# Kernel tuning notes

Measured on AMD Instinct MI355X. Metric: run time of the kernel, lower is better.

The kernel has to match this reference:

```python
import jax, jax.numpy as jnp
import numpy as np

BIG = 1e10  # sentinel for invalid pairwise distances


def get_xyz(depth, fx, fy, cx, cy):
    # depth: [B,1,H,W] -> xyz: [B,3,H,W] via pinhole unprojection
    B, _, H, W = depth.shape
    v = jnp.arange(H, dtype=depth.dtype)[:, None]   # rows
    u = jnp.arange(W, dtype=depth.dtype)[None, :]   # cols
    z = depth[:, 0]                                  # [B,H,W]
    x = (u - cx) / fx * z
    y = (v - cy) / fy * z
    return jnp.stack([x, y, z], axis=1)              # [B,3,H,W]


def _chamfer_item(p, g, vp, vg):
    # p,g: [N,3] point sets; vp,vg: [N] bool validity masks
    # squared pairwise distances via ||p||^2 + ||g||^2 - 2 p.g
    d = (jnp.sum(p * p, -1)[:, None] + jnp.sum(g * g, -1)[None, :]
         - 2.0 * (p @ g.T))                          # [N,N]
    d = jnp.maximum(d, 0.0)
    has_g = jnp.any(vg)
    has_p = jnp.any(vp)
    d1 = jnp.min(jnp.where(vg[None, :], d, BIG), axis=1)  # per pred point
    d2 = jnp.min(jnp.where(vp[:, None], d, BIG), axis=0)  # per gt point
    s1 = jnp.sum(jnp.where(vp & has_g, d1, 0.0))
    s2 = jnp.sum(jnp.where(vg & has_p, d2, 0.0))
    return s1 + s2


def reference(pred, gt_xyz, mask, fx, fy, cx, cy):
    B = pred.shape[0]
    pred_xyz = get_xyz(pred, fx, fy, cx, cy)             # [B,3,H,W]
    p = pred_xyz.reshape(B, 3, -1).transpose(0, 2, 1)    # [B,N,3]
    g = gt_xyz.reshape(B, 3, -1).transpose(0, 2, 1)      # [B,N,3]
    m = mask[:, 0].reshape(B, -1) > 0                    # [B,N]
    # ignore_zeros=True: drop points whose coordinate sum is exactly 0
    vp = m & (jnp.sum(p, -1) != 0)
    vg = m & (jnp.sum(g, -1) != 0)
    per_item = jax.vmap(_chamfer_item)(p, g, vp, vg)     # [B]
    return jnp.sum(per_item) / B


def setup_inputs() -> dict:
    key = jax.random.key(0)
    k1, k2, k3 = jax.random.split(key, 3)
    B, H, W = 2, 128, 128
    pred = jax.random.uniform(k1, (B, 1, H, W), dtype=jnp.float32) * 2.0 + 0.1
    gt_xyz = jax.random.normal(k2, (B, 3, H, W), dtype=jnp.float32)
    mask = jax.random.randint(k3, (B, 1, H, W), 0, 2, dtype=jnp.int32)
    fx = jnp.float32(525.0)
    fy = jnp.float32(525.0)
    cx = jnp.float32(64.0)
    cy = jnp.float32(64.0)
    return {"pred": pred, "gt_xyz": gt_xyz, "mask": mask,
            "fx": fx, "fy": fy, "cx": cx, "cy": cy}
```

## Files before the change

kernel.cpp:

```cpp
#include <hip/hip_runtime.h>

#define B_ITEMS 2
#define W_IMG   128
#define N_PTS   16384
#define CH_GRID 1024

__global__ __launch_bounds__(256) void prep_kernel(
        const float* __restrict__ pred,
        const float* __restrict__ gt,
        const int*   __restrict__ mask,
        const float* fxp, const float* fyp,
        const float* cxp, const float* cyp,
        int*    __restrict__ cnt,
        float4* __restrict__ pR, float4* __restrict__ gR,
        float4* __restrict__ pT, float4* __restrict__ gT,
        float*  __restrict__ out) {
    int s    = blockIdx.x >> 6;
    int b    = s & 1;
    int isG  = s >> 1;
    int tid  = threadIdx.x;
    int idx  = (blockIdx.x & 63) * 256 + tid;
    int lane = tid & 63, w = tid >> 6;

    if (blockIdx.x == 0 && tid == 0) out[0] = 0.0f;

    float x, y, z;
    if (!isG) {
        float fx = *fxp, fy = *fyp, cx = *cxp, cy = *cyp;
        float u = (float)(idx & (W_IMG - 1));
        float v = (float)(idx >> 7);
        z = pred[b * N_PTS + idx];
        x = (u - cx) / fx * z;
        y = (v - cy) / fy * z;
    } else {
        x = gt[(b * 3 + 0) * N_PTS + idx];
        y = gt[(b * 3 + 1) * N_PTS + idx];
        z = gt[(b * 3 + 2) * N_PTS + idx];
    }
    int  mv = mask[b * N_PTS + idx];
    bool ok = (mv > 0) && (((x + y) + z) != 0.0f);

    unsigned long long bal = __ballot(ok);
    int nw  = __popcll(bal);
    int pre = __popcll(bal & ((1ull << lane) - 1ull));

    __shared__ int wbase[4];
    __shared__ int blockbase;
    if (lane == 0) wbase[w] = nw;
    __syncthreads();
    if (tid == 0) {
        int s0 = 0;
#pragma unroll
        for (int i = 0; i < 4; ++i) { int t = wbase[i]; wbase[i] = s0; s0 += t; }
        blockbase = s0 ? atomicAdd(&cnt[s], s0) : 0;
    }
    __syncthreads();

    if (ok) {
        int pos = blockbase + wbase[w] + pre;
        float ps = fmaf(z, z, fmaf(y, y, x * x));
        float4* __restrict__ raw = (isG ? gR : pR) + b * N_PTS;
        float4* __restrict__ tf  = (isG ? gT : pT) + b * N_PTS;
        raw[pos] = make_float4(x, y, z, ps);
        tf[pos]  = make_float4(-2.0f * x, -2.0f * y, -2.0f * z, ps);
    }
}

__global__ __launch_bounds__(256, 4) void chamfer_kernel(
        const int*    __restrict__ cnt,
        const float4* __restrict__ pR, const float4* __restrict__ gR,
        const float4* __restrict__ pT, const float4* __restrict__ gT,
        float* __restrict__ out) {
    int np0 = cnt[0], np1 = cnt[1], ng0 = cnt[2], ng1 = cnt[3];
    int naArr[4] = {np0, ng0, np1, ng1};
    int nbArr[4] = {ng0, np0, ng1, np1};
    const float4* Arow[4] = {pR, gR, pR + N_PTS, gR + N_PTS};
    const float4* Bcol[4] = {gT, pT, gT + N_PTS, pT + N_PTS};

    int units[4];
    int Utot = 0;
#pragma unroll
    for (int i = 0; i < 4; ++i) {
        units[i] = (naArr[i] > 0 && nbArr[i] > 0) ? ((naArr[i] + 63) >> 6) : 0;
        Utot += units[i];
    }
    int u = blockIdx.x;
    if (u >= Utot) return;
    int s = 0;
    while (u >= units[s]) { u -= units[s]; ++s; }
    int na = naArr[s], nb = nbArr[s];
    const float4* __restrict__ A  = Arow[s];
    const float4* __restrict__ Bp = Bcol[s];
    int rowbase = u * 64;

    int tid = threadIdx.x;
    int tc = tid & 31, tr = tid >> 5;

    float px[8], py[8], pz[8], rm[8];
#pragma unroll
    for (int a = 0; a < 8; ++a) {
        float4 v = A[rowbase + a * 8 + tr];
        px[a] = v.x; py[a] = v.y; pz[a] = v.z;
        rm[a] = 3.4e38f;
    }

    __shared__ float4 sB[2][256];
    __shared__ float  smin[64];
    int ntiles = (nb + 255) >> 8;

    {
        int j = tid;
        float4 v = Bp[min(j, N_PTS - 1)];
        bool okc = j < nb;
        float4 r;
        r.x = okc ? v.x : 0.0f;
        r.y = okc ? v.y : 0.0f;
        r.z = okc ? v.z : 0.0f;
        r.w = okc ? v.w : 3.4e38f;
        sB[0][tid] = r;
    }
    __syncthreads();

    for (int t = 0; t < ntiles; ++t) {
        float4 r;
        bool have = (t + 1 < ntiles);
        if (have) {
            int j = (t + 1) * 256 + tid;
            float4 v = Bp[min(j, N_PTS - 1)];
            bool okc = j < nb;
            r.x = okc ? v.x : 0.0f;
            r.y = okc ? v.y : 0.0f;
            r.z = okc ? v.z : 0.0f;
            r.w = okc ? v.w : 3.4e38f;
        }
        const float4* __restrict__ buf = sB[t & 1];
#pragma unroll
        for (int cb = 0; cb < 8; ++cb) {
            float4 c = buf[cb * 32 + tc];
#pragma unroll
            for (int a = 0; a < 8; ++a)
                rm[a] = fminf(rm[a],
                    fmaf(px[a], c.x, fmaf(py[a], c.y, fmaf(pz[a], c.z, c.w))));
        }
        if (have) sB[(t + 1) & 1][tid] = r;
        __syncthreads();
    }

#pragma unroll
    for (int a = 0; a < 8; ++a) {
        float v = rm[a];
        v = fminf(v, __shfl_xor(v, 1, 64));
        v = fminf(v, __shfl_xor(v, 2, 64));
        v = fminf(v, __shfl_xor(v, 4, 64));
        v = fminf(v, __shfl_xor(v, 8, 64));
        v = fminf(v, __shfl_xor(v, 16, 64));
        rm[a] = v;
    }
    if (tc == 0) {
#pragma unroll
        for (int a = 0; a < 8; ++a) smin[a * 8 + tr] = rm[a];
    }
    __syncthreads();
    if (tid < 64) {
        int row = rowbase + tid;
        float v  = smin[tid];
        float ps = A[row].w;
        float contrib = (row < na) ? fmaxf(v + ps, 0.0f) : 0.0f;
#pragma unroll
        for (int off = 32; off > 0; off >>= 1)
            contrib += __shfl_down(contrib, off, 64);
        if (tid == 0) atomicAdd(out, contrib * (1.0f / B_ITEMS));
    }
}

extern "C" void kernel_launch(void* const* d_in, const int* in_sizes, int n_in,
                              void* d_out, int out_size, void* d_ws, size_t ws_size,
                              hipStream_t stream) {
    const float* pred = (const float*)d_in[0];
    const float* gt   = (const float*)d_in[1];
    const int*   mask = (const int*)  d_in[2];
    const float* fx   = (const float*)d_in[3];
    const float* fy   = (const float*)d_in[4];
    const float* cx   = (const float*)d_in[5];
    const float* cy   = (const float*)d_in[6];
    float* out = (float*)d_out;

    char* ws = (char*)d_ws;
    size_t SEG = (size_t)B_ITEMS * N_PTS * 16;
    int*    cnt = (int*)ws;
    float4* pR  = (float4*)(ws + 256);
    float4* gR  = (float4*)(ws + 256 + SEG);
    float4* pT  = (float4*)(ws + 256 + 2 * SEG);
    float4* gT  = (float4*)(ws + 256 + 3 * SEG);

    hipMemsetAsync(cnt, 0, 16, stream);

    prep_kernel<<<dim3(256), 256, 0, stream>>>(
        pred, gt, mask, fx, fy, cx, cy, cnt, pR, gR, pT, gT, out);

    chamfer_kernel<<<dim3(CH_GRID), 256, 0, stream>>>(
        cnt, pR, gR, pT, gT, out);
}
```

Before: 104.2 us.

## Give each wave 16 rows over all 64 lanes and double the column tile

Each thread now holds 16 row points instead of 8, and the 64 lanes of a wave stride across the column tile, so each shared-memory load feeds twice as many FMA/min operations. The column tile grows to 512 points, which halves the number of tile iterations and barriers. The final reduction becomes per-wave, using shuffles and one atomic per wave in place of the shared-memory staging and block barrier. In exchange, register pressure rises with 16 rows of coordinates and minima per thread, there are four atomics per block, and loading all 16 rows from one address range per thread is less coalesced.

After: 122.2 us. +17.2%, slower.

```diff
diff --git a/kernel.cpp b/kernel.cpp
--- a/kernel.cpp
+++ b/kernel.cpp
@@ -93,23 +93,24 @@
     const float4* __restrict__ Bp = Bcol[s];
     int rowbase = u * 64;
 
-    int tid = threadIdx.x;
-    int tc = tid & 31, tr = tid >> 5;
-
-    float px[8], py[8], pz[8], rm[8];
-#pragma unroll
-    for (int a = 0; a < 8; ++a) {
-        float4 v = A[rowbase + a * 8 + tr];
+    int tid  = threadIdx.x;
+    int w    = tid >> 6;
+    int lane = tid & 63;
+
+    float px[16], py[16], pz[16], rm[16];
+#pragma unroll
+    for (int a = 0; a < 16; ++a) {
+        float4 v = A[rowbase + w * 16 + a];
         px[a] = v.x; py[a] = v.y; pz[a] = v.z;
         rm[a] = 3.4e38f;
     }
 
-    __shared__ float4 sB[2][256];
-    __shared__ float  smin[64];
-    int ntiles = (nb + 255) >> 8;
-
-    {
-        int j = tid;
+    __shared__ float4 sB[2][512];
+    int ntiles = (nb + 511) >> 9;
+
+#pragma unroll
+    for (int k = 0; k < 2; ++k) {
+        int j = k * 256 + tid;
         float4 v = Bp[min(j, N_PTS - 1)];
         bool okc = j < nb;
         float4 r;
@@ -117,60 +118,67 @@
         r.y = okc ? v.y : 0.0f;
         r.z = okc ? v.z : 0.0f;
         r.w = okc ? v.w : 3.4e38f;
-        sB[0][tid] = r;
+        sB[0][k * 256 + tid] = r;
     }
     __syncthreads();
 
     for (int t = 0; t < ntiles; ++t) {
-        float4 r;
+        float4 r0, r1;
         bool have = (t + 1 < ntiles);
         if (have) {
-            int j = (t + 1) * 256 + tid;
-            float4 v = Bp[min(j, N_PTS - 1)];
-            bool okc = j < nb;
-            r.x = okc ? v.x : 0.0f;
-            r.y = okc ? v.y : 0.0f;
-            r.z = okc ? v.z : 0.0f;
-            r.w = okc ? v.w : 3.4e38f;
+            int j0 = (t + 1) * 512 + tid;
+            int j1 = j0 + 256;
+            float4 v0 = Bp[min(j0, N_PTS - 1)];
+            float4 v1 = Bp[min(j1, N_PTS - 1)];
+            bool k0 = j0 < nb, k1 = j1 < nb;
+            r0.x = k0 ? v0.x : 0.0f; r0.y = k0 ? v0.y : 0.0f;
+            r0.z = k0 ? v0.z : 0.0f; r0.w = k0 ? v0.w : 3.4e38f;
+            r1.x = k1 ? v1.x : 0.0f; r1.y = k1 ? v1.y : 0.0f;
+            r1.z = k1 ? v1.z : 0.0f; r1.w = k1 ? v1.w : 3.4e38f;
         }
-        const float4* __restrict__ buf = sB[t & 1];
+        const float4* __restrict__ buf = sB[t & 1] + lane;
 #pragma unroll
         for (int cb = 0; cb < 8; ++cb) {
-            float4 c = buf[cb * 32 + tc];
-#pragma unroll
-            for (int a = 0; a < 8; ++a)
+            float4 c = buf[cb * 64];
+#pragma unroll
+            for (int a = 0; a < 16; ++a)
                 rm[a] = fminf(rm[a],
                     fmaf(px[a], c.x, fmaf(py[a], c.y, fmaf(pz[a], c.z, c.w))));
         }
-        if (have) sB[(t + 1) & 1][tid] = r;
+        if (have) {
+            sB[(t + 1) & 1][tid] = r0;
+            sB[(t + 1) & 1][256 + tid] = r1;
+        }
         __syncthreads();
     }
 
 #pragma unroll
-    for (int a = 0; a < 8; ++a) {
+    for (int a = 0; a < 16; ++a) {
         float v = rm[a];
         v = fminf(v, __shfl_xor(v, 1, 64));
         v = fminf(v, __shfl_xor(v, 2, 64));
         v = fminf(v, __shfl_xor(v, 4, 64));
         v = fminf(v, __shfl_xor(v, 8, 64));
         v = fminf(v, __shfl_xor(v, 16, 64));
+        v = fminf(v, __shfl_xor(v, 32, 64));
         rm[a] = v;
     }
-    if (tc == 0) {
-#pragma unroll
-        for (int a = 0; a < 8; ++a) smin[a * 8 + tr] = rm[a];
-    }
-    __syncthreads();
-    if (tid < 64) {
-        int row = rowbase + tid;
-        float v  = smin[tid];
+    float acc = 0.0f;
+#pragma unroll
+    for (int a = 0; a < 16; ++a)
+        acc = (lane == a) ? rm[a] : acc;
+    if (lane < 16) {
+        int row = rowbase + w * 16 + lane;
         float ps = A[row].w;
-        float contrib = (row < na) ? fmaxf(v + ps, 0.0f) : 0.0f;
-#pragma unroll
-        for (int off = 32; off > 0; off >>= 1)
-            contrib += __shfl_down(contrib, off, 64);
-        if (tid == 0) atomicAdd(out, contrib * (1.0f / B_ITEMS));
-    }
+        acc = (row < na) ? fmaxf(acc + ps, 0.0f) : 0.0f;
+    } else {
+        acc = 0.0f;
+    }
+    acc += __shfl_xor(acc, 1, 64);
+    acc += __shfl_xor(acc, 2, 64);
+    acc += __shfl_xor(acc, 4, 64);
+    acc += __shfl_xor(acc, 8, 64);
+    if (lane == 0) atomicAdd(out, acc * (1.0f / B_ITEMS));
 }
 
 extern "C" void kernel_launch(void* const* d_in, const int* in_sizes, int n_in,
```
